# Performance work log

Measured on AMD Instinct MI355X. Metric: run time of the kernel, lower is better.

## Reference

```python
import jax, jax.numpy as jnp
from jax import lax
import numpy as np

IN, HID, NCLS, B, S = 360, 64, 5, 64, 128
MH_CONST = 2.0 / (np.sqrt(3.0) * np.pi ** 0.25)


def setup_inputs() -> dict:
    key = jax.random.key(0)
    ks = jax.random.split(key, 24)
    g = lambda i, shape, s=0.05: jax.random.normal(ks[i], shape, jnp.float32) * s
    inp = {
        'x_seq': jax.random.normal(ks[0], (B, S, IN), jnp.float32),
        # WavKANLinear params (out=64, in=360)
        'wav_scale': jnp.ones((HID, IN), jnp.float32),
        'wav_translation': jnp.zeros((HID, IN), jnp.float32),
        'wav_weights': g(1, (HID, IN)),
        'base_weight': g(2, (HID, IN)),
        # BatchNorm1d (eval mode, running stats)
        'bn_gamma': jnp.ones((HID,), jnp.float32),
        'bn_beta': jnp.zeros((HID,), jnp.float32),
        'bn_mean': jnp.zeros((HID,), jnp.float32),
        'bn_var': jnp.ones((HID,), jnp.float32),
        # LayerNorm(64)
        'ln_gamma': jnp.ones((HID,), jnp.float32),
        'ln_beta': jnp.zeros((HID,), jnp.float32),
        # bidirectional GRU, 1 layer, hidden=64
        'gru_w_ih_f': g(3, (3 * HID, HID)), 'gru_w_hh_f': g(4, (3 * HID, HID)),
        'gru_b_ih_f': g(5, (3 * HID,)), 'gru_b_hh_f': g(6, (3 * HID,)),
        'gru_w_ih_b': g(7, (3 * HID, HID)), 'gru_w_hh_b': g(8, (3 * HID, HID)),
        'gru_b_ih_b': g(9, (3 * HID,)), 'gru_b_hh_b': g(10, (3 * HID,)),
        # classifier: Linear(128,64) -> ReLU -> Linear(64,5)
        'fc1_w': g(11, (HID, 2 * HID)), 'fc1_b': jnp.zeros((HID,), jnp.float32),
        'fc2_w': g(12, (NCLS, HID)), 'fc2_b': jnp.zeros((NCLS,), jnp.float32),
    }
    return inp


def _gru_dir(x_sbf, w_ih, w_hh, b_ih, b_hh, reverse):
    # x_sbf: (S, B, F). Returns final hidden (B, H). PyTorch GRU equations.
    Bn = x_sbf.shape[1]
    H = w_hh.shape[1]
    gi_all = jnp.einsum('sbf,gf->sbg', x_sbf, w_ih) + b_ih  # precompute input gates

    def step(h, gi):
        gh = h @ w_hh.T + b_hh
        i_r, i_z, i_n = jnp.split(gi, 3, axis=-1)
        h_r, h_z, h_n = jnp.split(gh, 3, axis=-1)
        r = jax.nn.sigmoid(i_r + h_r)
        z = jax.nn.sigmoid(i_z + h_z)
        n = jnp.tanh(i_n + r * h_n)
        h_new = (1.0 - z) * n + z * h
        return h_new, None

    h0 = jnp.zeros((Bn, H), x_sbf.dtype)
    h_final, _ = lax.scan(step, h0, gi_all, reverse=reverse)
    return h_final


def reference(x_seq, wav_scale, wav_translation, wav_weights, base_weight,
              bn_gamma, bn_beta, bn_mean, bn_var, ln_gamma, ln_beta,
              gru_w_ih_f, gru_w_hh_f, gru_b_ih_f, gru_b_hh_f,
              gru_w_ih_b, gru_w_hh_b, gru_b_ih_b, gru_b_hh_b,
              fc1_w, fc1_b, fc2_w, fc2_b):
    b, s, f = x_seq.shape
    x_flat = x_seq.reshape(b * s, f)  # (N, 360)

    # --- WavKANLinear (mexican_hat) ---
    x_scaled = (x_flat[:, None, :] - wav_translation[None]) / wav_scale[None]  # (N, 64, 360)
    wavelet = MH_CONST * (x_scaled * x_scaled - 1.0) * jnp.exp(-0.5 * x_scaled * x_scaled)
    wav_out = jnp.einsum('noi,oi->no', wavelet, wav_weights)  # (N, 64)
    base_out = jax.nn.silu(x_flat) @ base_weight.T
    combined = wav_out + base_out
    # BatchNorm1d eval mode
    x_emb = (combined - bn_mean) * lax.rsqrt(bn_var + 1e-5) * bn_gamma + bn_beta

    # --- LayerNorm(64) ---
    mu = jnp.mean(x_emb, axis=-1, keepdims=True)
    var = jnp.mean(jnp.square(x_emb - mu), axis=-1, keepdims=True)
    x_emb = (x_emb - mu) * lax.rsqrt(var + 1e-5) * ln_gamma + ln_beta
    # dropout is identity in eval mode

    x_sbf = x_emb.reshape(b, s, HID).swapaxes(0, 1)  # (S, B, 64)

    # --- bidirectional GRU, take final hiddens ---
    h_fwd = _gru_dir(x_sbf, gru_w_ih_f, gru_w_hh_f, gru_b_ih_f, gru_b_hh_f, False)
    h_bwd = _gru_dir(x_sbf, gru_w_ih_b, gru_w_hh_b, gru_b_ih_b, gru_b_hh_b, True)
    hidden_cat = jnp.concatenate([h_fwd, h_bwd], axis=1)  # (B, 128)

    # --- classifier ---
    h = jax.nn.relu(hidden_cat @ fc1_w.T + fc1_b)
    logits = h @ fc2_w.T + fc2_b
    return logits
```

## Files before the change

### kernel.cpp

```cpp
#include <hip/hip_runtime.h>

#define IN_F   360
#define HIDN   64
#define NCLS   5
#define BATCH  64
#define SEQ    128
#define NROWS  (BATCH*SEQ)

#define WS_FLAG  0
#define WS_WPACK 16
#define WS_WFAST 92176
#define WS_WT4   138256
#define WS_XEMB  162832
#define WS_GI    687120
#define WS_HC    3832848

#define LOG2E        1.4426950408889634f
#define NEG_HALF_L2E (-0.7213475204444817f)

__device__ __forceinline__ float fast_rcp(float x) { return __builtin_amdgcn_rcpf(x); }
__device__ __forceinline__ float fast_rsq(float x) { return __builtin_amdgcn_rsqf(x); }
__device__ __forceinline__ float sigmoid_(float x) {
    x = fminf(fmaxf(x, -60.0f), 60.0f);
    return fast_rcp(1.0f + exp2f(-LOG2E * x));
}
__device__ __forceinline__ float tanh_(float x) {
    x = fminf(fmaxf(x, -30.0f), 30.0f);
    float e = exp2f(-2.8853900817779268f * x);
    return (1.0f - e) * fast_rcp(1.0f + e);
}
__device__ __forceinline__ float readlane_f(float v, int l) {
    return __int_as_float(__builtin_amdgcn_readlane(__float_as_int(v), l));
}

__global__ __launch_bounds__(256) void prep_kernel(
    const float* __restrict__ scale, const float* __restrict__ trans,
    const float* __restrict__ ww,    const float* __restrict__ bw,
    const float* __restrict__ wihf,  const float* __restrict__ wihb,
    float* __restrict__ ws) {
    int idx = blockIdx.x * 256 + threadIdx.x;
    float4* wpack  = (float4*)(ws + WS_WPACK);
    float2* wfast2 = (float2*)(ws + WS_WFAST);
    float*  wT4    = ws + WS_WT4;
    int*    flagp  = (int*)(ws + WS_FLAG);
    if (idx < 64 * IN_F) {
        int o = idx & 63, i = idx >> 6;
        float s  = scale[o * IN_F + i];
        float tr = trans[o * IN_F + i];
        if (s != 1.0f || tr != 0.0f) atomicOr(flagp, 1);
        float a  = 1.0f / s;
        float b  = -tr * a;
        float wq = 0.8673250705840776f * ww[o * IN_F + i];
        float bb = bw[o * IN_F + i];
        wpack[i * 64 + o] = make_float4(a, b, wq, bb);
        wfast2[(i >> 1) * 128 + o * 2 + (i & 1)] = make_float2(wq, bb);
    }
    int idx2 = idx - 64 * IN_F;
    if (idx2 >= 0 && idx2 < 24576) {
        int e = idx2 & 3; int rest = idx2 >> 2;
        int g = rest % 384; int k4 = rest / 384;
        int k = k4 * 4 + e; int dir = g / 192; int gg = g - dir * 192;
        const float* src = dir ? wihb : wihf;
        wT4[idx2] = src[gg * 64 + k];
    }
}

__global__ __launch_bounds__(256) void wavkan_kernel(
    const float* __restrict__ x_seq,
    const float* __restrict__ bn_g, const float* __restrict__ bn_b,
    const float* __restrict__ bn_m, const float* __restrict__ bn_v,
    const float* __restrict__ ln_g, const float* __restrict__ ln_b,
    const float* __restrict__ ws_c, float* __restrict__ x_emb) {
    __shared__ float2 xs_lds[16 * IN_F];
    int t = threadIdx.x;
    int row0 = blockIdx.x * 16;
    int o = t & 63, grp = t >> 6;
    int fast = (*(const int*)(ws_c + WS_FLAG)) == 0;

    float acc0 = 0.f, acc1 = 0.f, acc2 = 0.f, acc3 = 0.f;

    if (fast) {
        for (int idx = t; idx < 16 * IN_F; idx += 256) {
            int r = idx / IN_F, i = idx - r * IN_F;
            float x = x_seq[(row0 + r) * IN_F + i];
            float u = x * x;
            float phi = (u - 1.0f) * exp2f(u * NEG_HALF_L2E);
            float sl  = x * fast_rcp(1.0f + exp2f(-LOG2E * x));
            xs_lds[idx] = make_float2(phi, sl);
        }
        __syncthreads();
        const float4* wf4 = (const float4*)(ws_c + WS_WFAST);
        const float4* xs4 = (const float4*)xs_lds;
        const float4* xr0 = xs4 + (grp * 4 + 0) * 180;
        const float4* xr1 = xs4 + (grp * 4 + 1) * 180;
        const float4* xr2 = xs4 + (grp * 4 + 2) * 180;
        const float4* xr3 = xs4 + (grp * 4 + 3) * 180;
        #pragma unroll 2
        for (int i2 = 0; i2 < 180; ++i2) {
            float4 wp = wf4[i2 * 64 + o];
            float4 a = xr0[i2];
            acc0 = fmaf(a.x, wp.x, acc0); acc0 = fmaf(a.y, wp.y, acc0);
            acc0 = fmaf(a.z, wp.z, acc0); acc0 = fmaf(a.w, wp.w, acc0);
            float4 b = xr1[i2];
            acc1 = fmaf(b.x, wp.x, acc1); acc1 = fmaf(b.y, wp.y, acc1);
            acc1 = fmaf(b.z, wp.z, acc1); acc1 = fmaf(b.w, wp.w, acc1);
            float4 c = xr2[i2];
            acc2 = fmaf(c.x, wp.x, acc2); acc2 = fmaf(c.y, wp.y, acc2);
            acc2 = fmaf(c.z, wp.z, acc2); acc2 = fmaf(c.w, wp.w, acc2);
            float4 d = xr3[i2];
            acc3 = fmaf(d.x, wp.x, acc3); acc3 = fmaf(d.y, wp.y, acc3);
            acc3 = fmaf(d.z, wp.z, acc3); acc3 = fmaf(d.w, wp.w, acc3);
        }
    } else {
        for (int idx = t; idx < 16 * IN_F; idx += 256) {
            int r = idx / IN_F, i = idx - r * IN_F;
            float x = x_seq[(row0 + r) * IN_F + i];
            float sl = x * fast_rcp(1.0f + exp2f(-LOG2E * x));
            xs_lds[idx] = make_float2(x, sl);
        }
        __syncthreads();
        const float4* wpack = (const float4*)(ws_c + WS_WPACK);
        const float2* xr0 = xs_lds + (grp * 4 + 0) * IN_F;
        const float2* xr1 = xs_lds + (grp * 4 + 1) * IN_F;
        const float2* xr2 = xs_lds + (grp * 4 + 2) * IN_F;
        const float2* xr3 = xs_lds + (grp * 4 + 3) * IN_F;
        for (int i = 0; i < IN_F; ++i) {
            float4 wp = wpack[i * 64 + o];
            {
                float2 xs = xr0[i];
                float xsc = fmaf(xs.x, wp.x, wp.y); float u = xsc * xsc;
                float e = exp2f(u * NEG_HALF_L2E);
                acc0 = fmaf((u - 1.0f) * e, wp.z, acc0);
                acc0 = fmaf(xs.y, wp.w, acc0);
            }
            {
                float2 xs = xr1[i];
                float xsc = fmaf(xs.x, wp.x, wp.y); float u = xsc * xsc;
                float e = exp2f(u * NEG_HALF_L2E);
                acc1 = fmaf((u - 1.0f) * e, wp.z, acc1);
                acc1 = fmaf(xs.y, wp.w, acc1);
            }
            {
                float2 xs = xr2[i];
                float xsc = fmaf(xs.x, wp.x, wp.y); float u = xsc * xsc;
                float e = exp2f(u * NEG_HALF_L2E);
                acc2 = fmaf((u - 1.0f) * e, wp.z, acc2);
                acc2 = fmaf(xs.y, wp.w, acc2);
            }
            {
                float2 xs = xr3[i];
                float xsc = fmaf(xs.x, wp.x, wp.y); float u = xsc * xsc;
                float e = exp2f(u * NEG_HALF_L2E);
                acc3 = fmaf((u - 1.0f) * e, wp.z, acc3);
                acc3 = fmaf(xs.y, wp.w, acc3);
            }
        }
    }

    float bscale = bn_g[o] * fast_rsq(bn_v[o] + 1e-5f);
    float bshift = fmaf(-bn_m[o], bscale, bn_b[o]);
    float lg = ln_g[o], lb = ln_b[o];
    float vals[4] = {acc0, acc1, acc2, acc3};
    #pragma unroll
    for (int rr = 0; rr < 4; ++rr) {
        float y = fmaf(vals[rr], bscale, bshift);
        float s = y;
        #pragma unroll
        for (int m = 1; m < 64; m <<= 1) s += __shfl_xor(s, m, 64);
        float mu = s * (1.0f / 64.0f);
        float d = y - mu;
        float s2 = d * d;
        #pragma unroll
        for (int m = 1; m < 64; m <<= 1) s2 += __shfl_xor(s2, m, 64);
        float rstd = fast_rsq(s2 * (1.0f / 64.0f) + 1e-5f);
        x_emb[(row0 + grp * 4 + rr) * 64 + o] = fmaf(d * rstd, lg, lb);
    }
}

__global__ __launch_bounds__(384) void gi_kernel(
    const float* __restrict__ ws_c,
    const float* __restrict__ bihf, const float* __restrict__ bihb,
    float* __restrict__ gi) {
    __shared__ __align__(16) float xs[32 * 64];
    const float4* wT4   = (const float4*)(ws_c + WS_WT4);
    const float*  x_emb = ws_c + WS_XEMB;
    int t = threadIdx.x;
    int row0 = blockIdx.x * 32;
    {
        const float4* src = (const float4*)(x_emb + row0 * 64);
        float4* dst = (float4*)xs;
        for (int i = t; i < 512; i += 384) dst[i] = src[i];
    }
    int dir = t / 192, gg = t - dir * 192;
    float bih = dir ? bihb[gg] : bihf[gg];
    float4 w[16];
    #pragma unroll
    for (int k4 = 0; k4 < 16; ++k4) w[k4] = wT4[k4 * 384 + t];
    __syncthreads();
    for (int r = 0; r < 32; r += 2) {
        const float4* x0 = (const float4*)(xs + r * 64);
        const float4* x1 = (const float4*)(xs + r * 64 + 64);
        float a0 = bih, a1 = 0.f, b0 = bih, b1 = 0.f;
        #pragma unroll
        for (int k4 = 0; k4 < 16; k4 += 2) {
            float4 xv = x0[k4];     float4 wv = w[k4];
            a0 = fmaf(xv.x, wv.x, a0); a0 = fmaf(xv.y, wv.y, a0);
            a0 = fmaf(xv.z, wv.z, a0); a0 = fmaf(xv.w, wv.w, a0);
            float4 xu = x0[k4 + 1]; float4 wu = w[k4 + 1];
            a1 = fmaf(xu.x, wu.x, a1); a1 = fmaf(xu.y, wu.y, a1);
            a1 = fmaf(xu.z, wu.z, a1); a1 = fmaf(xu.w, wu.w, a1);
            float4 yv = x1[k4];
            b0 = fmaf(yv.x, wv.x, b0); b0 = fmaf(yv.y, wv.y, b0);
            b0 = fmaf(yv.z, wv.z, b0); b0 = fmaf(yv.w, wv.w, b0);
            float4 yu = x1[k4 + 1];
            b1 = fmaf(yu.x, wu.x, b1); b1 = fmaf(yu.y, wu.y, b1);
            b1 = fmaf(yu.z, wu.z, b1); b1 = fmaf(yu.w, wu.w, b1);
        }
        gi[(row0 + r) * 384 + t]     = a0 + a1;
        gi[(row0 + r + 1) * 384 + t] = b0 + b1;
    }
}

__global__ __launch_bounds__(192, 1) void gru_kernel(
    const float* __restrict__ ws_c,
    const float* __restrict__ whhf, const float* __restrict__ bhhf,
    const float* __restrict__ whhb, const float* __restrict__ bhhb,
    float* __restrict__ hc) {
    __shared__ __align__(16) float gi_l[64 * 192];
    __shared__ float gh[2][192];
    const float* gi = ws_c + WS_GI;
    int t = threadIdx.x, lane = t & 63;
    int b = blockIdx.x & 63, dir = blockIdx.x >> 6;
    const float* whh = dir ? whhb : whhf;
    const float* bhh = dir ? bhhb : bhhf;

    float w[64];
    {
        const float4* wrow = (const float4*)(whh + t * 64);
        #pragma unroll
        for (int q = 0; q < 16; ++q) {
            float4 a = wrow[q];
            w[4*q] = a.x; w[4*q+1] = a.y; w[4*q+2] = a.z; w[4*q+3] = a.w;
        }
    }
    float bias = bhh[t];

    const float* gsrc = gi + (size_t)(b * SEQ) * 384 + dir * 192 + t;
    #pragma unroll
    for (int q = 0; q < 64; ++q) {
        int sidx = dir ? (SEQ - 1 - q) : q;
        gi_l[q * 192 + t] = gsrc[sidx * 384];
    }
    float pf[64];
    #pragma unroll
    for (int q = 0; q < 64; ++q) {
        int sidx = dir ? (SEQ - 1 - (64 + q)) : (64 + q);
        pf[q] = gsrc[sidx * 384];
    }
    float hreg = 0.0f;
    __syncthreads();

    for (int ss = 0; ss < SEQ; ++ss) {
        if (ss == 64) {
            __syncthreads();
            #pragma unroll
            for (int q = 0; q < 64; ++q) gi_l[q * 192 + t] = pf[q];
            __syncthreads();
        }
        int ssl = ss & 63;
        float a0 = bias, a1 = 0.f, a2 = 0.f, a3 = 0.f;
        #pragma unroll
        for (int k = 0; k < 64; k += 4) {
            float h0 = readlane_f(hreg, k);
            float h1 = readlane_f(hreg, k + 1);
            float h2 = readlane_f(hreg, k + 2);
            float h3 = readlane_f(hreg, k + 3);
            a0 = fmaf(w[k],     h0, a0);
            a1 = fmaf(w[k + 1], h1, a1);
            a2 = fmaf(w[k + 2], h2, a2);
            a3 = fmaf(w[k + 3], h3, a3);
        }
        int p = ss & 1;
        gh[p][t] = (a0 + a1) + (a2 + a3);
        float ir  = gi_l[ssl * 192 + lane];
        float iz  = gi_l[ssl * 192 + 64 + lane];
        float in_ = gi_l[ssl * 192 + 128 + lane];
        __syncthreads();
        float r = sigmoid_(ir + gh[p][lane]);
        float z = sigmoid_(iz + gh[p][64 + lane]);
        float n = tanh_(fmaf(r, gh[p][128 + lane], in_));
        hreg = fmaf(z, hreg - n, n);
    }
    if (t < 64) hc[b * 128 + dir * 64 + lane] = hreg;
}

__global__ __launch_bounds__(64) void head_kernel(
    const float* __restrict__ ws_c,
    const float* __restrict__ fc1w, const float* __restrict__ fc1b,
    const float* __restrict__ fc2w, const float* __restrict__ fc2b,
    float* __restrict__ out) {
    __shared__ __align__(16) float hr[128];
    __shared__ float h1[64];
    const float* hc = ws_c + WS_HC;
    int bb = blockIdx.x, t = threadIdx.x;
    hr[t]      = hc[bb * 128 + t];
    hr[64 + t] = hc[bb * 128 + 64 + t];
    __syncthreads();
    float acc = fc1b[t];
    const float4* w4 = (const float4*)(fc1w + t * 128);
    const float4* h4 = (const float4*)hr;
    #pragma unroll 8
    for (int k4 = 0; k4 < 32; ++k4) {
        float4 wv = w4[k4]; float4 hv = h4[k4];
        acc = fmaf(hv.x, wv.x, acc); acc = fmaf(hv.y, wv.y, acc);
        acc = fmaf(hv.z, wv.z, acc); acc = fmaf(hv.w, wv.w, acc);
    }
    h1[t] = fmaxf(acc, 0.0f);
    __syncthreads();
    if (t < NCLS) {
        float acc2 = fc2b[t];
        const float* wr = fc2w + t * 64;
        #pragma unroll 8
        for (int k = 0; k < 64; ++k) acc2 = fmaf(h1[k], wr[k], acc2);
        out[bb * NCLS + t] = acc2;
    }
}

extern "C" void kernel_launch(void* const* d_in, const int* in_sizes, int n_in,
                              void* d_out, int out_size, void* d_ws, size_t ws_size,
                              hipStream_t stream) {
    const float* x_seq = (const float*)d_in[0];
    const float* wscal = (const float*)d_in[1];
    const float* wtran = (const float*)d_in[2];
    const float* wwght = (const float*)d_in[3];
    const float* bwght = (const float*)d_in[4];
    const float* bn_g  = (const float*)d_in[5];
    const float* bn_b  = (const float*)d_in[6];
    const float* bn_m  = (const float*)d_in[7];
    const float* bn_v  = (const float*)d_in[8];
    const float* ln_g  = (const float*)d_in[9];
    const float* ln_b  = (const float*)d_in[10];
    const float* wihf  = (const float*)d_in[11];
    const float* whhf  = (const float*)d_in[12];
    const float* bihf  = (const float*)d_in[13];
    const float* bhhf  = (const float*)d_in[14];
    const float* wihb  = (const float*)d_in[15];
    const float* whhb  = (const float*)d_in[16];
    const float* bihb  = (const float*)d_in[17];
    const float* bhhb  = (const float*)d_in[18];
    const float* fc1w  = (const float*)d_in[19];
    const float* fc1b  = (const float*)d_in[20];
    const float* fc2w  = (const float*)d_in[21];
    const float* fc2b  = (const float*)d_in[22];
    float* ws  = (float*)d_ws;
    float* out = (float*)d_out;

    hipMemsetAsync(ws + WS_FLAG, 0, sizeof(int), stream);
    hipLaunchKernelGGL(prep_kernel, dim3(186), dim3(256), 0, stream,
                       wscal, wtran, wwght, bwght, wihf, wihb, ws);
    hipLaunchKernelGGL(wavkan_kernel, dim3(NROWS / 16), dim3(256), 0, stream,
                       x_seq, bn_g, bn_b, bn_m, bn_v, ln_g, ln_b, ws, ws + WS_XEMB);
    hipLaunchKernelGGL(gi_kernel, dim3(NROWS / 32), dim3(384), 0, stream,
                       ws, bihf, bihb, ws + WS_GI);
    hipLaunchKernelGGL(gru_kernel, dim3(128), dim3(192), 0, stream,
                       ws, whhf, bhhf, whhb, bhhb, ws + WS_HC);
    hipLaunchKernelGGL(head_kernel, dim3(64), dim3(64), 0, stream,
                       ws, fc1w, fc1b, fc2w, fc2b, out);
}
```

Before: 224.3 us.

## Fuse all pipeline stages into one cooperative persistent kernel with grid syncs

Replaces the five separate launches (prep, WavKAN, input-gate GEMM, GRU recurrence, head) with a single cooperative kernel of 256 blocks that separates stages with grid.sync(). Each block now handles two WavKAN tiles and a re-tiled gi computation with 256 threads. The aim is to remove per-kernel launch overhead and the gaps between dependent kernels. The cost is fewer threads per stage, with the GRU and head phases leaving most blocks idle. The fused kernel is also limited to one block per CU with a large shared-memory footprint, which may reduce throughput in the WavKAN phase.

Result: slower. 402.1 us (+79.3%).

```diff
diff --git a/kernel.cpp b/kernel.cpp
--- a/kernel.cpp
+++ b/kernel.cpp
@@ -1,4 +1,7 @@
 #include <hip/hip_runtime.h>
+#include <hip/hip_cooperative_groups.h>
+
+namespace cg = cooperative_groups;
 
 #define IN_F   360
 #define HIDN   64
@@ -33,337 +36,349 @@
     return __int_as_float(__builtin_amdgcn_readlane(__float_as_int(v), l));
 }
 
-__global__ __launch_bounds__(256) void prep_kernel(
-    const float* __restrict__ scale, const float* __restrict__ trans,
-    const float* __restrict__ ww,    const float* __restrict__ bw,
-    const float* __restrict__ wihf,  const float* __restrict__ wihb,
-    float* __restrict__ ws) {
-    int idx = blockIdx.x * 256 + threadIdx.x;
-    float4* wpack  = (float4*)(ws + WS_WPACK);
-    float2* wfast2 = (float2*)(ws + WS_WFAST);
-    float*  wT4    = ws + WS_WT4;
-    int*    flagp  = (int*)(ws + WS_FLAG);
-    if (idx < 64 * IN_F) {
-        int o = idx & 63, i = idx >> 6;
-        float s  = scale[o * IN_F + i];
-        float tr = trans[o * IN_F + i];
-        if (s != 1.0f || tr != 0.0f) atomicOr(flagp, 1);
-        float a  = 1.0f / s;
-        float b  = -tr * a;
-        float wq = 0.8673250705840776f * ww[o * IN_F + i];
-        float bb = bw[o * IN_F + i];
-        wpack[i * 64 + o] = make_float4(a, b, wq, bb);
-        wfast2[(i >> 1) * 128 + o * 2 + (i & 1)] = make_float2(wq, bb);
-    }
-    int idx2 = idx - 64 * IN_F;
-    if (idx2 >= 0 && idx2 < 24576) {
-        int e = idx2 & 3; int rest = idx2 >> 2;
-        int g = rest % 384; int k4 = rest / 384;
-        int k = k4 * 4 + e; int dir = g / 192; int gg = g - dir * 192;
-        const float* src = dir ? wihb : wihf;
-        wT4[idx2] = src[gg * 64 + k];
-    }
-}
-
-__global__ __launch_bounds__(256) void wavkan_kernel(
-    const float* __restrict__ x_seq,
-    const float* __restrict__ bn_g, const float* __restrict__ bn_b,
-    const float* __restrict__ bn_m, const float* __restrict__ bn_v,
-    const float* __restrict__ ln_g, const float* __restrict__ ln_b,
-    const float* __restrict__ ws_c, float* __restrict__ x_emb) {
-    __shared__ float2 xs_lds[16 * IN_F];
-    int t = threadIdx.x;
-    int row0 = blockIdx.x * 16;
-    int o = t & 63, grp = t >> 6;
-    int fast = (*(const int*)(ws_c + WS_FLAG)) == 0;
-
-    float acc0 = 0.f, acc1 = 0.f, acc2 = 0.f, acc3 = 0.f;
-
-    if (fast) {
-        for (int idx = t; idx < 16 * IN_F; idx += 256) {
-            int r = idx / IN_F, i = idx - r * IN_F;
-            float x = x_seq[(row0 + r) * IN_F + i];
-            float u = x * x;
-            float phi = (u - 1.0f) * exp2f(u * NEG_HALF_L2E);
-            float sl  = x * fast_rcp(1.0f + exp2f(-LOG2E * x));
-            xs_lds[idx] = make_float2(phi, sl);
-        }
-        __syncthreads();
-        const float4* wf4 = (const float4*)(ws_c + WS_WFAST);
-        const float4* xs4 = (const float4*)xs_lds;
-        const float4* xr0 = xs4 + (grp * 4 + 0) * 180;
-        const float4* xr1 = xs4 + (grp * 4 + 1) * 180;
-        const float4* xr2 = xs4 + (grp * 4 + 2) * 180;
-        const float4* xr3 = xs4 + (grp * 4 + 3) * 180;
-        #pragma unroll 2
-        for (int i2 = 0; i2 < 180; ++i2) {
-            float4 wp = wf4[i2 * 64 + o];
-            float4 a = xr0[i2];
-            acc0 = fmaf(a.x, wp.x, acc0); acc0 = fmaf(a.y, wp.y, acc0);
-            acc0 = fmaf(a.z, wp.z, acc0); acc0 = fmaf(a.w, wp.w, acc0);
-            float4 b = xr1[i2];
-            acc1 = fmaf(b.x, wp.x, acc1); acc1 = fmaf(b.y, wp.y, acc1);
-            acc1 = fmaf(b.z, wp.z, acc1); acc1 = fmaf(b.w, wp.w, acc1);
-            float4 c = xr2[i2];
-            acc2 = fmaf(c.x, wp.x, acc2); acc2 = fmaf(c.y, wp.y, acc2);
-            acc2 = fmaf(c.z, wp.z, acc2); acc2 = fmaf(c.w, wp.w, acc2);
-            float4 d = xr3[i2];
-            acc3 = fmaf(d.x, wp.x, acc3); acc3 = fmaf(d.y, wp.y, acc3);
-            acc3 = fmaf(d.z, wp.z, acc3); acc3 = fmaf(d.w, wp.w, acc3);
-        }
-    } else {
-        for (int idx = t; idx < 16 * IN_F; idx += 256) {
-            int r = idx / IN_F, i = idx - r * IN_F;
-            float x = x_seq[(row0 + r) * IN_F + i];
-            float sl = x * fast_rcp(1.0f + exp2f(-LOG2E * x));
-            xs_lds[idx] = make_float2(x, sl);
-        }
-        __syncthreads();
-        const float4* wpack = (const float4*)(ws_c + WS_WPACK);
-        const float2* xr0 = xs_lds + (grp * 4 + 0) * IN_F;
-        const float2* xr1 = xs_lds + (grp * 4 + 1) * IN_F;
-        const float2* xr2 = xs_lds + (grp * 4 + 2) * IN_F;
-        const float2* xr3 = xs_lds + (grp * 4 + 3) * IN_F;
-        for (int i = 0; i < IN_F; ++i) {
-            float4 wp = wpack[i * 64 + o];
-            {
-                float2 xs = xr0[i];
-                float xsc = fmaf(xs.x, wp.x, wp.y); float u = xsc * xsc;
-                float e = exp2f(u * NEG_HALF_L2E);
-                acc0 = fmaf((u - 1.0f) * e, wp.z, acc0);
-                acc0 = fmaf(xs.y, wp.w, acc0);
-            }
-            {
-                float2 xs = xr1[i];
-                float xsc = fmaf(xs.x, wp.x, wp.y); float u = xsc * xsc;
-                float e = exp2f(u * NEG_HALF_L2E);
-                acc1 = fmaf((u - 1.0f) * e, wp.z, acc1);
-                acc1 = fmaf(xs.y, wp.w, acc1);
-            }
-            {
-                float2 xs = xr2[i];
-                float xsc = fmaf(xs.x, wp.x, wp.y); float u = xsc * xsc;
-                float e = exp2f(u * NEG_HALF_L2E);
-                acc2 = fmaf((u - 1.0f) * e, wp.z, acc2);
-                acc2 = fmaf(xs.y, wp.w, acc2);
-            }
-            {
-                float2 xs = xr3[i];
-                float xsc = fmaf(xs.x, wp.x, wp.y); float u = xsc * xsc;
-                float e = exp2f(u * NEG_HALF_L2E);
-                acc3 = fmaf((u - 1.0f) * e, wp.z, acc3);
-                acc3 = fmaf(xs.y, wp.w, acc3);
-            }
-        }
-    }
-
-    float bscale = bn_g[o] * fast_rsq(bn_v[o] + 1e-5f);
-    float bshift = fmaf(-bn_m[o], bscale, bn_b[o]);
-    float lg = ln_g[o], lb = ln_b[o];
-    float vals[4] = {acc0, acc1, acc2, acc3};
-    #pragma unroll
-    for (int rr = 0; rr < 4; ++rr) {
-        float y = fmaf(vals[rr], bscale, bshift);
-        float s = y;
+struct Params {
+    const float *x_seq, *scale, *trans, *ww, *bw;
+    const float *bn_g, *bn_b, *bn_m, *bn_v, *ln_g, *ln_b;
+    const float *wihf, *whhf, *bihf, *bhhf;
+    const float *wihb, *whhb, *bihb, *bhhb;
+    const float *fc1w, *fc1b, *fc2w, *fc2b;
+    float *ws, *out;
+};
+
+__global__ __launch_bounds__(256, 1) void fused_kernel(Params p) {
+    cg::grid_group grid = cg::this_grid();
+    __shared__ __align__(16) float smem[12672];
+    int t = threadIdx.x, blk = blockIdx.x;
+    float* ws = p.ws;
+
+    {
+        int idx = blk * 256 + t;
+        float4* wpack  = (float4*)(ws + WS_WPACK);
+        float2* wfast2 = (float2*)(ws + WS_WFAST);
+        float*  wT4    = ws + WS_WT4;
+        int*    flagp  = (int*)(ws + WS_FLAG);
+        if (idx < 64 * IN_F) {
+            int o = idx & 63, i = idx >> 6;
+            float s  = p.scale[o * IN_F + i];
+            float tr = p.trans[o * IN_F + i];
+            if (s != 1.0f || tr != 0.0f) atomicOr(flagp, 1);
+            float a  = 1.0f / s;
+            float b  = -tr * a;
+            float wq = 0.8673250705840776f * p.ww[o * IN_F + i];
+            float bb = p.bw[o * IN_F + i];
+            wpack[i * 64 + o] = make_float4(a, b, wq, bb);
+            wfast2[(i >> 1) * 128 + o * 2 + (i & 1)] = make_float2(wq, bb);
+        }
+        int idx2 = idx - 64 * IN_F;
+        if (idx2 >= 0 && idx2 < 24576) {
+            int e = idx2 & 3; int rest = idx2 >> 2;
+            int g = rest % 384; int k4 = rest / 384;
+            int k = k4 * 4 + e; int dir = g / 192; int gg = g - dir * 192;
+            const float* src = dir ? p.wihb : p.wihf;
+            wT4[idx2] = src[gg * 64 + k];
+        }
+    }
+    grid.sync();
+
+    {
+        float2* xs_lds = (float2*)smem;
+        int o = t & 63, grp = t >> 6;
+        int fast = (*(const int*)(ws + WS_FLAG)) == 0;
+        float* x_emb = ws + WS_XEMB;
+        for (int it = 0; it < 2; ++it) {
+            int row0 = (blk + 256 * it) * 16;
+            float acc0 = 0.f, acc1 = 0.f, acc2 = 0.f, acc3 = 0.f;
+            if (fast) {
+                for (int idx = t; idx < 16 * IN_F; idx += 256) {
+                    int r = idx / IN_F, i = idx - r * IN_F;
+                    float x = p.x_seq[(row0 + r) * IN_F + i];
+                    float u = x * x;
+                    float phi = (u - 1.0f) * exp2f(u * NEG_HALF_L2E);
+                    float sl  = x * fast_rcp(1.0f + exp2f(-LOG2E * x));
+                    xs_lds[idx] = make_float2(phi, sl);
+                }
+                __syncthreads();
+                const float4* wf4 = (const float4*)(ws + WS_WFAST);
+                const float4* xs4 = (const float4*)xs_lds;
+                const float4* xr0 = xs4 + (grp * 4 + 0) * 180;
+                const float4* xr1 = xs4 + (grp * 4 + 1) * 180;
+                const float4* xr2 = xs4 + (grp * 4 + 2) * 180;
+                const float4* xr3 = xs4 + (grp * 4 + 3) * 180;
+                #pragma unroll 2
+                for (int i2 = 0; i2 < 180; ++i2) {
+                    float4 wp = wf4[i2 * 64 + o];
+                    float4 a = xr0[i2];
+                    acc0 = fmaf(a.x, wp.x, acc0); acc0 = fmaf(a.y, wp.y, acc0);
+                    acc0 = fmaf(a.z, wp.z, acc0); acc0 = fmaf(a.w, wp.w, acc0);
+                    float4 b = xr1[i2];
+                    acc1 = fmaf(b.x, wp.x, acc1); acc1 = fmaf(b.y, wp.y, acc1);
+                    acc1 = fmaf(b.z, wp.z, acc1); acc1 = fmaf(b.w, wp.w, acc1);
+                    float4 c = xr2[i2];
+                    acc2 = fmaf(c.x, wp.x, acc2); acc2 = fmaf(c.y, wp.y, acc2);
+                    acc2 = fmaf(c.z, wp.z, acc2); acc2 = fmaf(c.w, wp.w, acc2);
+                    float4 d = xr3[i2];
+                    acc3 = fmaf(d.x, wp.x, acc3); acc3 = fmaf(d.y, wp.y, acc3);
+                    acc3 = fmaf(d.z, wp.z, acc3); acc3 = fmaf(d.w, wp.w, acc3);
+                }
+            } else {
+                for (int idx = t; idx < 16 * IN_F; idx += 256) {
+                    int r = idx / IN_F, i = idx - r * IN_F;
+                    float x = p.x_seq[(row0 + r) * IN_F + i];
+                    float sl = x * fast_rcp(1.0f + exp2f(-LOG2E * x));
+                    xs_lds[idx] = make_float2(x, sl);
+                }
+                __syncthreads();
+                const float4* wpack = (const float4*)(ws + WS_WPACK);
+                const float2* xr0 = xs_lds + (grp * 4 + 0) * IN_F;
+                const float2* xr1 = xs_lds + (grp * 4 + 1) * IN_F;
+                const float2* xr2 = xs_lds + (grp * 4 + 2) * IN_F;
+                const float2* xr3 = xs_lds + (grp * 4 + 3) * IN_F;
+                for (int i = 0; i < IN_F; ++i) {
+                    float4 wp = wpack[i * 64 + o];
+                    {
+                        float2 xs = xr0[i];
+                        float xsc = fmaf(xs.x, wp.x, wp.y); float u = xsc * xsc;
+                        float e = exp2f(u * NEG_HALF_L2E);
+                        acc0 = fmaf((u - 1.0f) * e, wp.z, acc0);
+                        acc0 = fmaf(xs.y, wp.w, acc0);
+                    }
+                    {
+                        float2 xs = xr1[i];
+                        float xsc = fmaf(xs.x, wp.x, wp.y); float u = xsc * xsc;
+                        float e = exp2f(u * NEG_HALF_L2E);
+                        acc1 = fmaf((u - 1.0f) * e, wp.z, acc1);
+                        acc1 = fmaf(xs.y, wp.w, acc1);
+                    }
+                    {
+                        float2 xs = xr2[i];
+                        float xsc = fmaf(xs.x, wp.x, wp.y); float u = xsc * xsc;
+                        float e = exp2f(u * NEG_HALF_L2E);
+                        acc2 = fmaf((u - 1.0f) * e, wp.z, acc2);
+                        acc2 = fmaf(xs.y, wp.w, acc2);
+                    }
+                    {
+                        float2 xs = xr3[i];
+                        float xsc = fmaf(xs.x, wp.x, wp.y); float u = xsc * xsc;
+                        float e = exp2f(u * NEG_HALF_L2E);
+                        acc3 = fmaf((u - 1.0f) * e, wp.z, acc3);
+                        acc3 = fmaf(xs.y, wp.w, acc3);
+                    }
+                }
+            }
+            float bscale = p.bn_g[o] * fast_rsq(p.bn_v[o] + 1e-5f);
+            float bshift = fmaf(-p.bn_m[o], bscale, p.bn_b[o]);
+            float lg = p.ln_g[o], lb = p.ln_b[o];
+            float vals[4] = {acc0, acc1, acc2, acc3};
+            #pragma unroll
+            for (int rr = 0; rr < 4; ++rr) {
+                float y = fmaf(vals[rr], bscale, bshift);
+                float s = y;
+                #pragma unroll
+                for (int m = 1; m < 64; m <<= 1) s += __shfl_xor(s, m, 64);
+                float mu = s * (1.0f / 64.0f);
+                float d = y - mu;
+                float s2 = d * d;
+                #pragma unroll
+                for (int m = 1; m < 64; m <<= 1) s2 += __shfl_xor(s2, m, 64);
+                float rstd = fast_rsq(s2 * (1.0f / 64.0f) + 1e-5f);
+                x_emb[(row0 + grp * 4 + rr) * 64 + o] = fmaf(d * rstd, lg, lb);
+            }
+            __syncthreads();
+        }
+    }
+    grid.sync();
+
+    {
+        float* xs = smem;
+        const float4* wT4   = (const float4*)(ws + WS_WT4);
+        const float*  x_emb = ws + WS_XEMB;
+        float* gi = ws + WS_GI;
+        int row0 = blk * 32;
+        {
+            const float4* src = (const float4*)(x_emb + row0 * 64);
+            float4* dst = (float4*)xs;
+            dst[t] = src[t]; dst[t + 256] = src[t + 256];
+        }
+        int g1 = t;
+        float bih1 = (g1 < 192) ? p.bihf[g1] : p.bihb[g1 - 192];
+        float bih2 = (t < 128) ? p.bihb[64 + t] : 0.0f;
+        float4 w1[16], w2[16];
         #pragma unroll
-        for (int m = 1; m < 64; m <<= 1) s += __shfl_xor(s, m, 64);
-        float mu = s * (1.0f / 64.0f);
-        float d = y - mu;
-        float s2 = d * d;
-        #pragma unroll
-        for (int m = 1; m < 64; m <<= 1) s2 += __shfl_xor(s2, m, 64);
-        float rstd = fast_rsq(s2 * (1.0f / 64.0f) + 1e-5f);
-        x_emb[(row0 + grp * 4 + rr) * 64 + o] = fmaf(d * rstd, lg, lb);
-    }
-}
-
-__global__ __launch_bounds__(384) void gi_kernel(
-    const float* __restrict__ ws_c,
-    const float* __restrict__ bihf, const float* __restrict__ bihb,
-    float* __restrict__ gi) {
-    __shared__ __align__(16) float xs[32 * 64];
-    const float4* wT4   = (const float4*)(ws_c + WS_WT4);
-    const float*  x_emb = ws_c + WS_XEMB;
-    int t = threadIdx.x;
-    int row0 = blockIdx.x * 32;
-    {
-        const float4* src = (const float4*)(x_emb + row0 * 64);
-        float4* dst = (float4*)xs;
-        for (int i = t; i < 512; i += 384) dst[i] = src[i];
-    }
-    int dir = t / 192, gg = t - dir * 192;
-    float bih = dir ? bihb[gg] : bihf[gg];
-    float4 w[16];
-    #pragma unroll
-    for (int k4 = 0; k4 < 16; ++k4) w[k4] = wT4[k4 * 384 + t];
-    __syncthreads();
-    for (int r = 0; r < 32; r += 2) {
-        const float4* x0 = (const float4*)(xs + r * 64);
-        const float4* x1 = (const float4*)(xs + r * 64 + 64);
-        float a0 = bih, a1 = 0.f, b0 = bih, b1 = 0.f;
-        #pragma unroll
-        for (int k4 = 0; k4 < 16; k4 += 2) {
-            float4 xv = x0[k4];     float4 wv = w[k4];
-            a0 = fmaf(xv.x, wv.x, a0); a0 = fmaf(xv.y, wv.y, a0);
-            a0 = fmaf(xv.z, wv.z, a0); a0 = fmaf(xv.w, wv.w, a0);
-            float4 xu = x0[k4 + 1]; float4 wu = w[k4 + 1];
-            a1 = fmaf(xu.x, wu.x, a1); a1 = fmaf(xu.y, wu.y, a1);
-            a1 = fmaf(xu.z, wu.z, a1); a1 = fmaf(xu.w, wu.w, a1);
-            float4 yv = x1[k4];
-            b0 = fmaf(yv.x, wv.x, b0); b0 = fmaf(yv.y, wv.y, b0);
-            b0 = fmaf(yv.z, wv.z, b0); b0 = fmaf(yv.w, wv.w, b0);
-            float4 yu = x1[k4 + 1];
-            b1 = fmaf(yu.x, wu.x, b1); b1 = fmaf(yu.y, wu.y, b1);
-            b1 = fmaf(yu.z, wu.z, b1); b1 = fmaf(yu.w, wu.w, b1);
-        }
-        gi[(row0 + r) * 384 + t]     = a0 + a1;
-        gi[(row0 + r + 1) * 384 + t] = b0 + b1;
-    }
-}
-
-__global__ __launch_bounds__(192, 1) void gru_kernel(
-    const float* __restrict__ ws_c,
-    const float* __restrict__ whhf, const float* __restrict__ bhhf,
-    const float* __restrict__ whhb, const float* __restrict__ bhhb,
-    float* __restrict__ hc) {
-    __shared__ __align__(16) float gi_l[64 * 192];
-    __shared__ float gh[2][192];
-    const float* gi = ws_c + WS_GI;
-    int t = threadIdx.x, lane = t & 63;
-    int b = blockIdx.x & 63, dir = blockIdx.x >> 6;
-    const float* whh = dir ? whhb : whhf;
-    const float* bhh = dir ? bhhb : bhhf;
-
-    float w[64];
-    {
-        const float4* wrow = (const float4*)(whh + t * 64);
-        #pragma unroll
-        for (int q = 0; q < 16; ++q) {
-            float4 a = wrow[q];
-            w[4*q] = a.x; w[4*q+1] = a.y; w[4*q+2] = a.z; w[4*q+3] = a.w;
-        }
-    }
-    float bias = bhh[t];
-
-    const float* gsrc = gi + (size_t)(b * SEQ) * 384 + dir * 192 + t;
-    #pragma unroll
-    for (int q = 0; q < 64; ++q) {
-        int sidx = dir ? (SEQ - 1 - q) : q;
-        gi_l[q * 192 + t] = gsrc[sidx * 384];
-    }
-    float pf[64];
-    #pragma unroll
-    for (int q = 0; q < 64; ++q) {
-        int sidx = dir ? (SEQ - 1 - (64 + q)) : (64 + q);
-        pf[q] = gsrc[sidx * 384];
-    }
-    float hreg = 0.0f;
-    __syncthreads();
-
-    for (int ss = 0; ss < SEQ; ++ss) {
-        if (ss == 64) {
+        for (int k4 = 0; k4 < 16; ++k4) w1[k4] = wT4[k4 * 384 + g1];
+        if (t < 128) {
+            #pragma unroll
+            for (int k4 = 0; k4 < 16; ++k4) w2[k4] = wT4[k4 * 384 + 256 + t];
+        }
+        __syncthreads();
+        for (int r = 0; r < 32; ++r) {
+            const float4* x0 = (const float4*)(xs + r * 64);
+            float a0 = bih1, a1 = 0.f;
+            #pragma unroll
+            for (int k4 = 0; k4 < 16; k4 += 2) {
+                float4 xv = x0[k4];     float4 wv = w1[k4];
+                a0 = fmaf(xv.x, wv.x, a0); a0 = fmaf(xv.y, wv.y, a0);
+                a0 = fmaf(xv.z, wv.z, a0); a0 = fmaf(xv.w, wv.w, a0);
+                float4 xu = x0[k4 + 1]; float4 wu = w1[k4 + 1];
+                a1 = fmaf(xu.x, wu.x, a1); a1 = fmaf(xu.y, wu.y, a1);
+                a1 = fmaf(xu.z, wu.z, a1); a1 = fmaf(xu.w, wu.w, a1);
+            }
+            gi[(row0 + r) * 384 + g1] = a0 + a1;
+            if (t < 128) {
+                float b0 = bih2, b1 = 0.f;
+                #pragma unroll
+                for (int k4 = 0; k4 < 16; k4 += 2) {
+                    float4 xv = x0[k4];     float4 wv = w2[k4];
+                    b0 = fmaf(xv.x, wv.x, b0); b0 = fmaf(xv.y, wv.y, b0);
+                    b0 = fmaf(xv.z, wv.z, b0); b0 = fmaf(xv.w, wv.w, b0);
+                    float4 xu = x0[k4 + 1]; float4 wu = w2[k4 + 1];
+                    b1 = fmaf(xu.x, wu.x, b1); b1 = fmaf(xu.y, wu.y, b1);
+                    b1 = fmaf(xu.z, wu.z, b1); b1 = fmaf(xu.w, wu.w, b1);
+                }
+                gi[(row0 + r) * 384 + 256 + t] = b0 + b1;
+            }
+        }
+        __syncthreads();
+    }
+    grid.sync();
+
+    if (blk < 128) {
+        float* gi_l = smem;
+        float* ghb  = smem + 12288;
+        const float* gi = ws + WS_GI;
+        int lane = t & 63;
+        int b = blk & 63, dir = blk >> 6;
+        const float* whh = dir ? p.whhb : p.whhf;
+        const float* bhh = dir ? p.bhhb : p.bhhf;
+
+        float w[64];
+        float bias = 0.0f;
+        float pf[64];
+        float hreg = 0.0f;
+        if (t < 192) {
+            const float4* wrow = (const float4*)(whh + t * 64);
+            #pragma unroll
+            for (int q = 0; q < 16; ++q) {
+                float4 a = wrow[q];
+                w[4*q] = a.x; w[4*q+1] = a.y; w[4*q+2] = a.z; w[4*q+3] = a.w;
+            }
+            bias = bhh[t];
+            const float* gsrc = gi + (size_t)(b * SEQ) * 384 + dir * 192 + t;
+            #pragma unroll
+            for (int q = 0; q < 64; ++q) {
+                int sidx = dir ? (SEQ - 1 - q) : q;
+                gi_l[q * 192 + t] = gsrc[sidx * 384];
+            }
+            #pragma unroll
+            for (int q = 0; q < 64; ++q) {
+                int sidx = dir ? (SEQ - 1 - (64 + q)) : (64 + q);
+                pf[q] = gsrc[sidx * 384];
+            }
+        }
+        __syncthreads();
+
+        for (int ss = 0; ss < SEQ; ++ss) {
+            if (ss == 64) {
+                __syncthreads();
+                if (t < 192) {
+                    #pragma unroll
+                    for (int q = 0; q < 64; ++q) gi_l[q * 192 + t] = pf[q];
+                }
+                __syncthreads();
+            }
+            int ssl = ss & 63;
+            int pp = ss & 1;
+            float ir = 0.f, iz = 0.f, in_ = 0.f;
+            if (t < 192) {
+                float a0 = bias, a1 = 0.f, a2 = 0.f, a3 = 0.f;
+                #pragma unroll
+                for (int k = 0; k < 64; k += 4) {
+                    float h0 = readlane_f(hreg, k);
+                    float h1 = readlane_f(hreg, k + 1);
+                    float h2 = readlane_f(hreg, k + 2);
+                    float h3 = readlane_f(hreg, k + 3);
+                    a0 = fmaf(w[k],     h0, a0);
+                    a1 = fmaf(w[k + 1], h1, a1);
+                    a2 = fmaf(w[k + 2], h2, a2);
+                    a3 = fmaf(w[k + 3], h3, a3);
+                }
+                ghb[pp * 192 + t] = (a0 + a1) + (a2 + a3);
+                ir  = gi_l[ssl * 192 + lane];
+                iz  = gi_l[ssl * 192 + 64 + lane];
+                in_ = gi_l[ssl * 192 + 128 + lane];
+            }
             __syncthreads();
-            #pragma unroll
-            for (int q = 0; q < 64; ++q) gi_l[q * 192 + t] = pf[q];
-            __syncthreads();
-        }
-        int ssl = ss & 63;
-        float a0 = bias, a1 = 0.f, a2 = 0.f, a3 = 0.f;
-        #pragma unroll
-        for (int k = 0; k < 64; k += 4) {
-            float h0 = readlane_f(hreg, k);
-            float h1 = readlane_f(hreg, k + 1);
-            float h2 = readlane_f(hreg, k + 2);
-            float h3 = readlane_f(hreg, k + 3);
-            a0 = fmaf(w[k],     h0, a0);
-            a1 = fmaf(w[k + 1], h1, a1);
-            a2 = fmaf(w[k + 2], h2, a2);
-            a3 = fmaf(w[k + 3], h3, a3);
-        }
-        int p = ss & 1;
-        gh[p][t] = (a0 + a1) + (a2 + a3);
-        float ir  = gi_l[ssl * 192 + lane];
-        float iz  = gi_l[ssl * 192 + 64 + lane];
-        float in_ = gi_l[ssl * 192 + 128 + lane];
-        __syncthreads();
-        float r = sigmoid_(ir + gh[p][lane]);
-        float z = sigmoid_(iz + gh[p][64 + lane]);
-        float n = tanh_(fmaf(r, gh[p][128 + lane], in_));
-        hreg = fmaf(z, hreg - n, n);
-    }
-    if (t < 64) hc[b * 128 + dir * 64 + lane] = hreg;
-}
-
-__global__ __launch_bounds__(64) void head_kernel(
-    const float* __restrict__ ws_c,
-    const float* __restrict__ fc1w, const float* __restrict__ fc1b,
-    const float* __restrict__ fc2w, const float* __restrict__ fc2b,
-    float* __restrict__ out) {
-    __shared__ __align__(16) float hr[128];
-    __shared__ float h1[64];
-    const float* hc = ws_c + WS_HC;
-    int bb = blockIdx.x, t = threadIdx.x;
-    hr[t]      = hc[bb * 128 + t];
-    hr[64 + t] = hc[bb * 128 + 64 + t];
-    __syncthreads();
-    float acc = fc1b[t];
-    const float4* w4 = (const float4*)(fc1w + t * 128);
-    const float4* h4 = (const float4*)hr;
-    #pragma unroll 8
-    for (int k4 = 0; k4 < 32; ++k4) {
-        float4 wv = w4[k4]; float4 hv = h4[k4];
-        acc = fmaf(hv.x, wv.x, acc); acc = fmaf(hv.y, wv.y, acc);
-        acc = fmaf(hv.z, wv.z, acc); acc = fmaf(hv.w, wv.w, acc);
-    }
-    h1[t] = fmaxf(acc, 0.0f);
-    __syncthreads();
-    if (t < NCLS) {
-        float acc2 = fc2b[t];
-        const float* wr = fc2w + t * 64;
-        #pragma unroll 8
-        for (int k = 0; k < 64; ++k) acc2 = fmaf(h1[k], wr[k], acc2);
-        out[bb * NCLS + t] = acc2;
+            if (t < 192) {
+                float r = sigmoid_(ir + ghb[pp * 192 + lane]);
+                float z = sigmoid_(iz + ghb[pp * 192 + 64 + lane]);
+                float n = tanh_(fmaf(r, ghb[pp * 192 + 128 + lane], in_));
+                hreg = fmaf(z, hreg - n, n);
+            }
+        }
+        if (t < 64) (ws + WS_HC)[b * 128 + dir * 64 + lane] = hreg;
+    }
+    grid.sync();
+
+    if (blk < 64) {
+        float* hr = smem;
+        float* h1 = smem + 128;
+        const float* hc = ws + WS_HC;
+        if (t < 128) hr[t] = hc[blk * 128 + t];
+        __syncthreads();
+        if (t < 64) {
+            float acc = p.fc1b[t];
+            const float4* w4 = (const float4*)(p.fc1w + t * 128);
+            const float4* h4 = (const float4*)hr;
+            #pragma unroll 8
+            for (int k4 = 0; k4 < 32; ++k4) {
+                float4 wv = w4[k4]; float4 hv = h4[k4];
+                acc = fmaf(hv.x, wv.x, acc); acc = fmaf(hv.y, wv.y, acc);
+                acc = fmaf(hv.z, wv.z, acc); acc = fmaf(hv.w, wv.w, acc);
+            }
+            h1[t] = fmaxf(acc, 0.0f);
+        }
+        __syncthreads();
+        if (t < NCLS) {
+            float acc2 = p.fc2b[t];
+            const float* wr = p.fc2w + t * 64;
+            #pragma unroll 8
+            for (int k = 0; k < 64; ++k) acc2 = fmaf(h1[k], wr[k], acc2);
+            p.out[blk * NCLS + t] = acc2;
+        }
     }
 }
 
 extern "C" void kernel_launch(void* const* d_in, const int* in_sizes, int n_in,
                               void* d_out, int out_size, void* d_ws, size_t ws_size,
                               hipStream_t stream) {
-    const float* x_seq = (const float*)d_in[0];
-    const float* wscal = (const float*)d_in[1];
-    const float* wtran = (const float*)d_in[2];
-    const float* wwght = (const float*)d_in[3];
-    const float* bwght = (const float*)d_in[4];
-    const float* bn_g  = (const float*)d_in[5];
-    const float* bn_b  = (const float*)d_in[6];
-    const float* bn_m  = (const float*)d_in[7];
-    const float* bn_v  = (const float*)d_in[8];
-    const float* ln_g  = (const float*)d_in[9];
-    const float* ln_b  = (const float*)d_in[10];
-    const float* wihf  = (const float*)d_in[11];
-    const float* whhf  = (const float*)d_in[12];
-    const float* bihf  = (const float*)d_in[13];
-    const float* bhhf  = (const float*)d_in[14];
-    const float* wihb  = (const float*)d_in[15];
-    const float* whhb  = (const float*)d_in[16];
-    const float* bihb  = (const float*)d_in[17];
-    const float* bhhb  = (const float*)d_in[18];
-    const float* fc1w  = (const float*)d_in[19];
-    const float* fc1b  = (const float*)d_in[20];
-    const float* fc2w  = (const float*)d_in[21];
-    const float* fc2b  = (const float*)d_in[22];
-    float* ws  = (float*)d_ws;
-    float* out = (float*)d_out;
-
-    hipMemsetAsync(ws + WS_FLAG, 0, sizeof(int), stream);
-    hipLaunchKernelGGL(prep_kernel, dim3(186), dim3(256), 0, stream,
-                       wscal, wtran, wwght, bwght, wihf, wihb, ws);
-    hipLaunchKernelGGL(wavkan_kernel, dim3(NROWS / 16), dim3(256), 0, stream,
-                       x_seq, bn_g, bn_b, bn_m, bn_v, ln_g, ln_b, ws, ws + WS_XEMB);
-    hipLaunchKernelGGL(gi_kernel, dim3(NROWS / 32), dim3(384), 0, stream,
-                       ws, bihf, bihb, ws + WS_GI);
-    hipLaunchKernelGGL(gru_kernel, dim3(128), dim3(192), 0, stream,
-                       ws, whhf, bhhf, whhb, bhhb, ws + WS_HC);
-    hipLaunchKernelGGL(head_kernel, dim3(64), dim3(64), 0, stream,
-                       ws, fc1w, fc1b, fc2w, fc2b, out);
-}
+    Params prm;
+    prm.x_seq = (const float*)d_in[0];
+    prm.scale = (const float*)d_in[1];
+    prm.trans = (const float*)d_in[2];
+    prm.ww    = (const float*)d_in[3];
+    prm.bw    = (const float*)d_in[4];
+    prm.bn_g  = (const float*)d_in[5];
+    prm.bn_b  = (const float*)d_in[6];
+    prm.bn_m  = (const float*)d_in[7];
+    prm.bn_v  = (const float*)d_in[8];
+    prm.ln_g  = (const float*)d_in[9];
+    prm.ln_b  = (const float*)d_in[10];
+    prm.wihf  = (const float*)d_in[11];
+    prm.whhf  = (const float*)d_in[12];
+    prm.bihf  = (const float*)d_in[13];
+    prm.bhhf  = (const float*)d_in[14];
+    prm.wihb  = (const float*)d_in[15];
+    prm.whhb  = (const float*)d_in[16];
+    prm.bihb  = (const float*)d_in[17];
+    prm.bhhb  = (const float*)d_in[18];
+    prm.fc1w  = (const float*)d_in[19];
+    prm.fc1b  = (const float*)d_in[20];
+    prm.fc2w  = (const float*)d_in[21];
+    prm.fc2b  = (const float*)d_in[22];
+    prm.ws    = (float*)d_ws;
+    prm.out   = (float*)d_out;
+
+    hipMemsetAsync((float*)d_ws + WS_FLAG, 0, sizeof(int), stream);
+    void* args[] = { &prm };
+    hipLaunchCooperativeKernel((void*)fused_kernel, dim3(256), dim3(256),
+                               args, 0, stream);
+}
```

## Process two batch rows per GRU block to share recurrent weights

Applied to the files above, without the earlier changes.

Each GRU block now handles two batch elements in the same direction, so one set of W_hh registers serves two matvecs per step. This halves the block count from 128 to 64 and gives each step two independent dependency chains to interleave. The gate-input staging becomes a rolling 32-step window refilled from a register prefetch every 32 steps, instead of two fixed halves of 64. The cost is roughly twice the per-step ALU and readlane work on each block, so the serial step latency may grow. Using fewer blocks also leaves most CUs idle.

Measured after the change: 282.1 us. 25.8% more time.

```diff
diff --git a/kernel.cpp b/kernel.cpp
--- a/kernel.cpp
+++ b/kernel.cpp
@@ -226,11 +226,12 @@
     const float* __restrict__ whhf, const float* __restrict__ bhhf,
     const float* __restrict__ whhb, const float* __restrict__ bhhb,
     float* __restrict__ hc) {
-    __shared__ __align__(16) float gi_l[64 * 192];
-    __shared__ float gh[2][192];
+    __shared__ __align__(16) float gi_l[32 * 384];
+    __shared__ float gh[2][384];
     const float* gi = ws_c + WS_GI;
     int t = threadIdx.x, lane = t & 63;
-    int b = blockIdx.x & 63, dir = blockIdx.x >> 6;
+    int dir = blockIdx.x >> 5;
+    int b0 = (blockIdx.x & 31) * 2, b1 = b0 + 1;
     const float* whh = dir ? whhb : whhf;
     const float* bhh = dir ? bhhb : bhhf;
 
@@ -245,53 +246,85 @@
     }
     float bias = bhh[t];
 
-    const float* gsrc = gi + (size_t)(b * SEQ) * 384 + dir * 192 + t;
+    const float* gsrc0 = gi + (size_t)(b0 * SEQ) * 384 + dir * 192 + t;
+    const float* gsrc1 = gi + (size_t)(b1 * SEQ) * 384 + dir * 192 + t;
+
     #pragma unroll
-    for (int q = 0; q < 64; ++q) {
+    for (int q = 0; q < 32; ++q) {
         int sidx = dir ? (SEQ - 1 - q) : q;
-        gi_l[q * 192 + t] = gsrc[sidx * 384];
-    }
-    float pf[64];
+        gi_l[q * 384 + t]       = gsrc0[sidx * 384];
+        gi_l[q * 384 + 192 + t] = gsrc1[sidx * 384];
+    }
+    float pf0[32], pf1[32];
     #pragma unroll
-    for (int q = 0; q < 64; ++q) {
-        int sidx = dir ? (SEQ - 1 - (64 + q)) : (64 + q);
-        pf[q] = gsrc[sidx * 384];
-    }
-    float hreg = 0.0f;
+    for (int q = 0; q < 32; ++q) {
+        int sidx = dir ? (SEQ - 1 - (32 + q)) : (32 + q);
+        pf0[q] = gsrc0[sidx * 384];
+        pf1[q] = gsrc1[sidx * 384];
+    }
+    float h0 = 0.0f, h1 = 0.0f;
     __syncthreads();
 
     for (int ss = 0; ss < SEQ; ++ss) {
-        if (ss == 64) {
+        int ssl = ss & 31;
+        if (ss != 0 && ssl == 0) {
             __syncthreads();
             #pragma unroll
-            for (int q = 0; q < 64; ++q) gi_l[q * 192 + t] = pf[q];
+            for (int q = 0; q < 32; ++q) {
+                gi_l[q * 384 + t]       = pf0[q];
+                gi_l[q * 384 + 192 + t] = pf1[q];
+            }
             __syncthreads();
-        }
-        int ssl = ss & 63;
+            if (ss < 96) {
+                #pragma unroll
+                for (int q = 0; q < 32; ++q) {
+                    int s_it = ss + 32 + q;
+                    int sidx = dir ? (SEQ - 1 - s_it) : s_it;
+                    pf0[q] = gsrc0[sidx * 384];
+                    pf1[q] = gsrc1[sidx * 384];
+                }
+            }
+        }
         float a0 = bias, a1 = 0.f, a2 = 0.f, a3 = 0.f;
+        float c0 = bias, c1 = 0.f, c2 = 0.f, c3 = 0.f;
         #pragma unroll
         for (int k = 0; k < 64; k += 4) {
-            float h0 = readlane_f(hreg, k);
-            float h1 = readlane_f(hreg, k + 1);
-            float h2 = readlane_f(hreg, k + 2);
-            float h3 = readlane_f(hreg, k + 3);
-            a0 = fmaf(w[k],     h0, a0);
-            a1 = fmaf(w[k + 1], h1, a1);
-            a2 = fmaf(w[k + 2], h2, a2);
-            a3 = fmaf(w[k + 3], h3, a3);
-        }
-        int p = ss & 1;
-        gh[p][t] = (a0 + a1) + (a2 + a3);
-        float ir  = gi_l[ssl * 192 + lane];
-        float iz  = gi_l[ssl * 192 + 64 + lane];
-        float in_ = gi_l[ssl * 192 + 128 + lane];
+            float x0 = readlane_f(h0, k);
+            float y0 = readlane_f(h1, k);
+            float x1 = readlane_f(h0, k + 1);
+            float y1 = readlane_f(h1, k + 1);
+            float x2 = readlane_f(h0, k + 2);
+            float y2 = readlane_f(h1, k + 2);
+            float x3 = readlane_f(h0, k + 3);
+            float y3 = readlane_f(h1, k + 3);
+            a0 = fmaf(w[k],     x0, a0); c0 = fmaf(w[k],     y0, c0);
+            a1 = fmaf(w[k + 1], x1, a1); c1 = fmaf(w[k + 1], y1, c1);
+            a2 = fmaf(w[k + 2], x2, a2); c2 = fmaf(w[k + 2], y2, c2);
+            a3 = fmaf(w[k + 3], x3, a3); c3 = fmaf(w[k + 3], y3, c3);
+        }
+        int pp = ss & 1;
+        gh[pp][t]       = (a0 + a1) + (a2 + a3);
+        gh[pp][192 + t] = (c0 + c1) + (c2 + c3);
+        float ir0 = gi_l[ssl * 384 + lane];
+        float iz0 = gi_l[ssl * 384 + 64 + lane];
+        float in0 = gi_l[ssl * 384 + 128 + lane];
+        float ir1 = gi_l[ssl * 384 + 192 + lane];
+        float iz1 = gi_l[ssl * 384 + 256 + lane];
+        float in1 = gi_l[ssl * 384 + 320 + lane];
         __syncthreads();
-        float r = sigmoid_(ir + gh[p][lane]);
-        float z = sigmoid_(iz + gh[p][64 + lane]);
-        float n = tanh_(fmaf(r, gh[p][128 + lane], in_));
-        hreg = fmaf(z, hreg - n, n);
-    }
-    if (t < 64) hc[b * 128 + dir * 64 + lane] = hreg;
+        float r0 = sigmoid_(ir0 + gh[pp][lane]);
+        float z0 = sigmoid_(iz0 + gh[pp][64 + lane]);
+        float n0 = tanh_(fmaf(r0, gh[pp][128 + lane], in0));
+        h0 = fmaf(z0, h0 - n0, n0);
+        float r1 = sigmoid_(ir1 + gh[pp][192 + lane]);
+        float z1 = sigmoid_(iz1 + gh[pp][256 + lane]);
+        float n1 = tanh_(fmaf(r1, gh[pp][320 + lane], in1));
+        h1 = fmaf(z1, h1 - n1, n1);
+    }
+    if (t < 64) {
+        hc[b0 * 128 + dir * 64 + lane] = h0;
+        hc[b1 * 128 + dir * 64 + lane] = h1;
+    }
 }
 
 __global__ __launch_bounds__(64) void head_kernel(
@@ -362,7 +395,7 @@
                        x_seq, bn_g, bn_b, bn_m, bn_v, ln_g, ln_b, ws, ws + WS_XEMB);
     hipLaunchKernelGGL(gi_kernel, dim3(NROWS / 32), dim3(384), 0, stream,
                        ws, bihf, bihb, ws + WS_GI);
-    hipLaunchKernelGGL(gru_kernel, dim3(128), dim3(192), 0, stream,
+    hipLaunchKernelGGL(gru_kernel, dim3(64), dim3(192), 0, stream,
                        ws, whhf, bhhf, whhb, bhhb, ws + WS_HC);
     hipLaunchKernelGGL(head_kernel, dim3(64), dim3(64), 0, stream,
                        ws, fc1w, fc1b, fc2w, fc2b, out);
```
